# Kernel optimization log

Measured on AMD Instinct MI355X. Metric: run time of the kernel, lower is better.

## Reference

```python
import jax, jax.numpy as jnp
from jax import lax
import numpy as np

CHI, CHO = 256, 256
B, H, W = 4, 64, 64
KH = KW = 3
K = KH * KW
EPS = 1e-5


def setup_inputs() -> dict:
    key = jax.random.key(0)
    ks = jax.random.split(key, 8)
    x = jax.random.normal(ks[0], (B, CHI, H, W), jnp.float32)
    # offset/mask conv: chi -> 3*K channels (dy[K], dx[K], mask[K]); small init so offsets stay local
    w_off = jax.random.normal(ks[1], (3 * K, CHI, KH, KW), jnp.float32) * 0.01
    b_off = jax.random.normal(ks[2], (3 * K,), jnp.float32) * 0.01
    weight = jax.random.normal(ks[3], (CHO, CHI, KH, KW), jnp.float32) * 0.05
    bias = jax.random.normal(ks[4], (CHO,), jnp.float32) * 0.05
    gamma = 1.0 + 0.1 * jax.random.normal(ks[5], (CHO,), jnp.float32)
    beta = 0.1 * jax.random.normal(ks[6], (CHO,), jnp.float32)
    rmean = 0.1 * jax.random.normal(ks[7], (CHO,), jnp.float32)
    rvar = jnp.ones((CHO,), jnp.float32)
    return {"x": x, "w_off": w_off, "b_off": b_off, "weight": weight,
            "bias": bias, "gamma": gamma, "beta": beta, "rmean": rmean, "rvar": rvar}


def _dcn_bn_relu(x, w_off, b_off, weight, bias, gamma, beta, rmean, rvar):
    Bn, C, Hn, Wn = x.shape
    cho = weight.shape[0]
    # offset/mask branch: ordinary 3x3 same conv
    om = lax.conv_general_dilated(x, w_off, (1, 1), ((1, 1), (1, 1)),
                                  dimension_numbers=("NCHW", "OIHW", "NCHW"))
    om = om + b_off[None, :, None, None]
    o1, o2, m = jnp.split(om, 3, axis=1)            # each [B,K,H,W]
    mask = jax.nn.sigmoid(m).transpose(0, 2, 3, 1)  # [B,H,W,K]
    dy = o1.transpose(0, 2, 3, 1)                   # [B,H,W,K]
    dx = o2.transpose(0, 2, 3, 1)
    # sampling coords: p = out_pos - pad + k*dil + offset (stride=1, pad=1, dil=1)
    ky = jnp.repeat(jnp.arange(KH, dtype=x.dtype) - 1.0, KW)  # [K]
    kx = jnp.tile(jnp.arange(KW, dtype=x.dtype) - 1.0, KH)
    py = jnp.arange(Hn, dtype=x.dtype)[None, :, None, None] + ky + dy  # [B,H,W,K]
    px = jnp.arange(Wn, dtype=x.dtype)[None, None, :, None] + kx + dx

    xt = x.transpose(0, 2, 3, 1)  # [B,H,W,C]
    y0 = jnp.floor(py)
    x0 = jnp.floor(px)
    ly = py - y0
    lx = px - x0
    y0i = y0.astype(jnp.int32)
    x0i = x0.astype(jnp.int32)

    def corner(yi, xi, w):
        valid = (yi >= 0) & (yi < Hn) & (xi >= 0) & (xi < Wn)
        yc = jnp.clip(yi, 0, Hn - 1)
        xc = jnp.clip(xi, 0, Wn - 1)
        v = jax.vmap(lambda img, a, b: img[a, b])(xt, yc, xc)  # [B,H,W,K,C]
        return v * (w * valid.astype(x.dtype))[..., None]

    val = (corner(y0i, x0i, (1 - ly) * (1 - lx))
           + corner(y0i, x0i + 1, (1 - ly) * lx)
           + corner(y0i + 1, x0i, ly * (1 - lx))
           + corner(y0i + 1, x0i + 1, ly * lx))  # [B,H,W,K,C]

    cols = val * mask[..., None]  # modulated columns [B,H,W,K,C]
    wk = weight.reshape(cho, weight.shape[1], K)  # [O,C,K]
    out = jnp.einsum("bhwkc,ock->bohw", cols, wk) + bias[None, :, None, None]
    # BatchNorm (eval: running stats) + ReLU
    inv = gamma * lax.rsqrt(rvar + EPS)
    out = out * inv[None, :, None, None] + (beta - rmean * inv)[None, :, None, None]
    return jax.nn.relu(out)


def reference(x, w_off, b_off, weight, bias, gamma, beta, rmean, rvar):
    return _dcn_bn_relu(x, w_off, b_off, weight, bias, gamma, beta, rmean, rvar)
```

## Files before the change

kernel.cpp:

```cpp
#include <hip/hip_runtime.h>
#include <math.h>

#define NH 64
#define NW 64
#define NB 4
#define CHI 256
#define CHO 256
#define XT_B (66 * 66 * 256)

typedef __attribute__((ext_vector_type(8))) short bf16x8;
typedef __attribute__((ext_vector_type(4))) float f32x4;

static __device__ __forceinline__ unsigned short f2bf(float f) {
    unsigned int u = __float_as_uint(f);
    u += 0x7fffu + ((u >> 16) & 1u);
    return (unsigned short)(u >> 16);
}
static __device__ __forceinline__ float bflo(unsigned int p) { return __uint_as_float(p << 16); }
static __device__ __forceinline__ float bfhi(unsigned int p) { return __uint_as_float(p & 0xffff0000u); }
static __device__ __forceinline__ unsigned int pkbf(float a, float b) {
    unsigned int r;
    asm("v_cvt_pk_bf16_f32 %0, %1, %2" : "=v"(r) : "v"(a), "v"(b));
    return r;
}

#define BAR_LGKM() asm volatile("s_waitcnt lgkmcnt(0)\n\ts_barrier" ::: "memory")


__global__ __launch_bounds__(256) void prep_all(const float* __restrict__ weight,
                                                const float* __restrict__ w_off,
                                                const float* __restrict__ x,
                                                unsigned short* __restrict__ wB,
                                                unsigned short* __restrict__ wOB,
                                                unsigned short* __restrict__ xT) {
    __shared__ unsigned short sT[64 * 134];
    int bid = blockIdx.x, tid = threadIdx.x;
    if (bid < 2304) {
        int idx = bid * 256 + tid;
        int kin = idx & 31, o = (idx >> 5) & 255, ks = idx >> 13;
        int cc = ks / 9, kt = ks - cc * 9;
        int c = cc * 32 + kin;
        wB[idx] = f2bf(weight[((size_t)o * CHI + c) * 9 + kt]);
    } else if (bid < 2592) {
        int idx = (bid - 2304) * 256 + tid;
        int kin = idx & 31, oc = (idx >> 5) & 31, ks = idx >> 10;
        int cc = ks / 9, kt = ks - cc * 9;
        int c = cc * 32 + kin;
        wOB[idx] = (oc < 27) ? f2bf(w_off[((size_t)oc * CHI + c) * 9 + kt])
                             : (unsigned short)0;
    } else if (bid < 3104) {
        int bid2 = bid - 2592;
        int b = bid2 >> 7, rem = bid2 & 127;
        int y = rem >> 1, chalf = rem & 1;
        int c0 = chalf * 128;
        for (int rep = 0; rep < 8; ++rep) {
            int idx = rep * 256 + tid;
            int c = idx >> 4, p4 = (idx & 15) * 4;
            const float* src = x + (((size_t)b * CHI + c0 + c) * 64 + y) * 64 + p4;
            float4 v = *(const float4*)src;
            sT[(p4 + 0) * 134 + c] = f2bf(v.x);
            sT[(p4 + 1) * 134 + c] = f2bf(v.y);
            sT[(p4 + 2) * 134 + c] = f2bf(v.z);
            sT[(p4 + 3) * 134 + c] = f2bf(v.w);
        }
        __syncthreads();
        unsigned int* dst = (unsigned int*)(xT + ((size_t)(b * 66 + y + 1) * 66 + 1) * 256)
                          + chalf * 64;
        for (int rep = 0; rep < 16; ++rep) {
            int idx = rep * 256 + tid;
            int px = idx >> 6, cu = idx & 63;
            unsigned int lo = sT[px * 134 + cu * 2];
            unsigned int hi = sT[px * 134 + cu * 2 + 1];
            dst[(size_t)px * 128 + cu] = lo | (hi << 16);
        }
    } else {
        int flat = (bid - 3104) * 256 + tid;
        int b = flat / 33280, r = flat - b * 33280;
        unsigned int* xtu = (unsigned int*)xT;
        size_t base = (size_t)b * 66 * 66 * 128;
        size_t idx;
        if (r < 8448) {
            idx = base + r;
        } else if (r < 16896) {
            idx = base + (size_t)65 * 66 * 128 + (r - 8448);
        } else {
            int rc = r - 16896;
            int side = rc >> 13;
            int row = 1 + ((rc & 8191) >> 7);
            int cu = rc & 127;
            idx = base + ((size_t)row * 66 + (side ? 65 : 0)) * 128 + cu;
        }
        xtu[idx] = 0;
    }
}

__global__ __launch_bounds__(512, 4) void dcn_fused(
        const unsigned short* __restrict__ xT,
        const unsigned short* __restrict__ wOB,
        const unsigned short* __restrict__ wB,
        const float* __restrict__ b_off,
        const float* __restrict__ bias, const float* __restrict__ gamma,
        const float* __restrict__ beta, const float* __restrict__ rmean,
        const float* __restrict__ rvar, float* __restrict__ out) {
    __shared__ __align__(16) unsigned char smem[33280];
    int4*   s_po = (int4*)smem;
    float4* s_cw = (float4*)(smem + 4608);
    unsigned short* sA = (unsigned short*)(smem + 9216);
    float* sOff = (float*)(smem + 9216);
    float (*sOut)[260] = (float(*)[260])smem;

    int id = blockIdx.x;
    int xcd = id & 7, sl = id >> 3;
    int b = xcd >> 1;
    int h = (xcd & 1) * 32 + (sl & 31);
    int pxbase = (sl >> 5) * 32;

    int tid = threadIdx.x;
    int lane = tid & 63, q = tid >> 6;
    int ln = lane & 15, lk = lane >> 4;
    int nb = q & 3, kh = q >> 2;

    const unsigned short* xTfull = xT + (size_t)b * XT_B;
    const bf16x8* wOBv = (const bf16x8*)wOB;
    const bf16x8* wBv  = (const bf16x8*)wB;

    {
        int omt = q & 1, ont = (q >> 1) & 1, okq = q >> 2;
        int opx = pxbase + omt * 16 + ln;
        int oposbase = (h + 1) * 66 + opx + 1;
        f32x4 oa0 = {0.f, 0.f, 0.f, 0.f}, oa1 = {0.f, 0.f, 0.f, 0.f};
        for (int cc = okq * 4; cc < okq * 4 + 4; ++cc) {
#pragma unroll
            for (int kt = 0; kt < 9; ++kt) {
                int pos = oposbase + (kt / 3 - 1) * 66 + (kt % 3 - 1);
                bf16x8 af = *(const bf16x8*)&xTfull[(size_t)pos * 256 + cc * 32 + lk * 8];
                bf16x8 bo = wOBv[((size_t)(cc * 9 + kt) * 32 + ont * 16 + ln) * 4 + lk];
                if (kt & 1) oa1 = __builtin_amdgcn_mfma_f32_16x16x32_bf16(af, bo, oa1, 0, 0, 0);
                else        oa0 = __builtin_amdgcn_mfma_f32_16x16x32_bf16(af, bo, oa0, 0, 0, 0);
            }
        }
#pragma unroll
        for (int r = 0; r < 4; ++r)
            sOff[(okq * 32 + omt * 16 + lk * 4 + r) * 33 + ont * 16 + ln] = oa0[r] + oa1[r];
    }
    BAR_LGKM();

    for (int p = tid; p < 288; p += 512) {
        int k = p >> 5, pwl = p & 31, pw = pxbase + pwl;
        float dy = sOff[pwl * 33 + k]        + sOff[(32 + pwl) * 33 + k]        + b_off[k];
        float dx = sOff[pwl * 33 + k + 9]    + sOff[(32 + pwl) * 33 + k + 9]    + b_off[k + 9];
        float mp = sOff[pwl * 33 + k + 18]   + sOff[(32 + pwl) * 33 + k + 18]   + b_off[k + 18];
        float mv = 1.f / (1.f + __expf(-mp));
        float py  = (float)h  + (float)(k / 3 - 1) + dy;
        float pxf = (float)pw + (float)(k % 3 - 1) + dx;
        float y0f = floorf(py), x0f = floorf(pxf);
        int y0 = (int)y0f, x0 = (int)x0f;
        float ly = py - y0f, lx = pxf - x0f;
        int y0c = min(max(y0, -1), 64), y1c = min(max(y0 + 1, -1), 64);
        int x0c = min(max(x0, -1), 64), x1c = min(max(x0 + 1, -1), 64);
        int ry0 = (y0c + 1) * 66, ry1 = (y1c + 1) * 66;
        s_po[p] = make_int4(ry0 + x0c + 1, ry0 + x1c + 1, ry1 + x0c + 1, ry1 + x1c + 1);
        s_cw[p] = make_float4((1.f - ly) * (1.f - lx) * mv, (1.f - ly) * lx * mv,
                              ly * (1.f - lx) * mv,         ly * lx * mv);
    }

    int cg8 = tid & 3, pxl = (tid >> 2) & 31, sl4 = tid >> 7;
    int khp = sl4 >> 1, ip = sl4 & 1;
    const unsigned short* xTb = xTfull + cg8 * 8;

    f32x4 zf = {0.f, 0.f, 0.f, 0.f};
    f32x4 acc[2][4] = {{zf, zf, zf, zf}, {zf, zf, zf, zf}};

    uint4 C00, C01, C10, C11;

#define LOADS(s) do { int s_ = (s); int cc_ = s_ / 9; int kt_ = s_ - cc_ * 9;  \
        int4 o4_ = s_po[kt_ * 32 + pxl];                                       \
        const unsigned short* cb_ = xTb + cc_ * 32;                            \
        C00 = *(const uint4*)(cb_ + (size_t)o4_.x * 256);                      \
        C01 = *(const uint4*)(cb_ + (size_t)o4_.y * 256);                      \
        C10 = *(const uint4*)(cb_ + (size_t)o4_.z * 256);                      \
        C11 = *(const uint4*)(cb_ + (size_t)o4_.w * 256);                      \
    } while (0)

#define WRITEA(s, buf) do { int s_ = (s); int kt_ = s_ - (s_ / 9) * 9;         \
        float4 w_ = s_cw[kt_ * 32 + pxl];                                      \
        uint4 pk_;                                                             \
        pk_.x = pkbf(w_.x*bflo(C00.x)+w_.y*bflo(C01.x)+w_.z*bflo(C10.x)+w_.w*bflo(C11.x), \
                     w_.x*bfhi(C00.x)+w_.y*bfhi(C01.x)+w_.z*bfhi(C10.x)+w_.w*bfhi(C11.x)); \
        pk_.y = pkbf(w_.x*bflo(C00.y)+w_.y*bflo(C01.y)+w_.z*bflo(C10.y)+w_.w*bflo(C11.y), \
                     w_.x*bfhi(C00.y)+w_.y*bfhi(C01.y)+w_.z*bfhi(C10.y)+w_.w*bfhi(C11.y)); \
        pk_.z = pkbf(w_.x*bflo(C00.z)+w_.y*bflo(C01.z)+w_.z*bflo(C10.z)+w_.w*bflo(C11.z), \
                     w_.x*bfhi(C00.z)+w_.y*bfhi(C01.z)+w_.z*bfhi(C10.z)+w_.w*bfhi(C11.z)); \
        pk_.w = pkbf(w_.x*bflo(C00.w)+w_.y*bflo(C01.w)+w_.z*bflo(C10.w)+w_.w*bflo(C11.w), \
                     w_.x*bfhi(C00.w)+w_.y*bfhi(C01.w)+w_.z*bfhi(C10.w)+w_.w*bfhi(C11.w)); \
        *(uint4*)&sA[(buf) * 1280 + pxl * 40 + cg8 * 8] = pk_;                 \
    } while (0)

    BAR_LGKM();

    LOADS(khp * 36 + ip);
    WRITEA(khp * 36 + ip, sl4);
    LOADS(khp * 36 + 2 + ip);
    bf16x8 bfE[4], bfO[4];
#pragma unroll
    for (int j = 0; j < 4; ++j) {
        bfE[j] = wBv[((size_t)(kh * 36 + 0) * 256 + nb * 64 + j * 16 + ln) * 4 + lk];
        bfO[j] = wBv[((size_t)(kh * 36 + 1) * 256 + nb * 64 + j * 16 + ln) * 4 + lk];
    }
    BAR_LGKM();

    for (int g = 0; g < 18; ++g) {
        if (g + 1 < 18) WRITEA(khp * 36 + 2 * (g + 1) + ip, ((g + 1) & 1) * 4 + sl4);
        if (g + 2 < 18) LOADS(khp * 36 + 2 * (g + 2) + ip);

        int bufb = (g & 1) * 4 + kh * 2;
        const unsigned short* pA0 = &sA[bufb * 1280];
        const unsigned short* pA1 = &sA[bufb * 1280 + 1280];
        bf16x8 a00 = *(const bf16x8*)&pA0[ln * 40 + lk * 8];
        bf16x8 a01 = *(const bf16x8*)&pA0[(16 + ln) * 40 + lk * 8];
        bf16x8 a10 = *(const bf16x8*)&pA1[ln * 40 + lk * 8];
        bf16x8 a11 = *(const bf16x8*)&pA1[(16 + ln) * 40 + lk * 8];

#pragma unroll
        for (int j = 0; j < 4; ++j) {
            acc[0][j] = __builtin_amdgcn_mfma_f32_16x16x32_bf16(a00, bfE[j], acc[0][j], 0, 0, 0);
            acc[1][j] = __builtin_amdgcn_mfma_f32_16x16x32_bf16(a01, bfE[j], acc[1][j], 0, 0, 0);
        }
        if (2 * g + 2 < 36) {
#pragma unroll
            for (int j = 0; j < 4; ++j)
                bfE[j] = wBv[((size_t)(kh * 36 + 2 * g + 2) * 256 + nb * 64 + j * 16 + ln) * 4 + lk];
        }
#pragma unroll
        for (int j = 0; j < 4; ++j) {
            acc[0][j] = __builtin_amdgcn_mfma_f32_16x16x32_bf16(a10, bfO[j], acc[0][j], 0, 0, 0);
            acc[1][j] = __builtin_amdgcn_mfma_f32_16x16x32_bf16(a11, bfO[j], acc[1][j], 0, 0, 0);
        }
        if (2 * g + 3 < 36) {
#pragma unroll
            for (int j = 0; j < 4; ++j)
                bfO[j] = wBv[((size_t)(kh * 36 + 2 * g + 3) * 256 + nb * 64 + j * 16 + ln) * 4 + lk];
        }
        BAR_LGKM();
    }
#undef LOADS
#undef WRITEA

    if (kh == 1) {
#pragma unroll
        for (int m = 0; m < 2; ++m)
#pragma unroll
            for (int j = 0; j < 4; ++j) {
                int oc = nb * 64 + j * 16 + ln;
#pragma unroll
                for (int r = 0; r < 4; ++r)
                    sOut[m * 16 + lk * 4 + r][oc] = acc[m][j][r];
            }
    }
    __syncthreads();
    if (kh == 0) {
#pragma unroll
        for (int j = 0; j < 4; ++j) {
            int oc = nb * 64 + j * 16 + ln;
            float inv = gamma[oc] * rsqrtf(rvar[oc] + 1e-5f);
            float sh  = beta[oc] - rmean[oc] * inv + bias[oc] * inv;
#pragma unroll
            for (int m = 0; m < 2; ++m) {
                int row = m * 16 + lk * 4;
                float4 rr;
                rr.x = fmaxf((acc[m][j][0] + sOut[row + 0][oc]) * inv + sh, 0.f);
                rr.y = fmaxf((acc[m][j][1] + sOut[row + 1][oc]) * inv + sh, 0.f);
                rr.z = fmaxf((acc[m][j][2] + sOut[row + 2][oc]) * inv + sh, 0.f);
                rr.w = fmaxf((acc[m][j][3] + sOut[row + 3][oc]) * inv + sh, 0.f);
                size_t oi = (((size_t)b * 256 + oc) * 64 + h) * 64 + pxbase + row;
                *(float4*)(out + oi) = rr;
            }
        }
    }
}

extern "C" void kernel_launch(void* const* d_in, const int* in_sizes, int n_in,
                              void* d_out, int out_size, void* d_ws, size_t ws_size,
                              hipStream_t stream) {
    const float* x      = (const float*)d_in[0];
    const float* w_off  = (const float*)d_in[1];
    const float* b_off  = (const float*)d_in[2];
    const float* weight = (const float*)d_in[3];
    const float* bias   = (const float*)d_in[4];
    const float* gamma  = (const float*)d_in[5];
    const float* beta   = (const float*)d_in[6];
    const float* rmean  = (const float*)d_in[7];
    const float* rvar   = (const float*)d_in[8];
    float* out = (float*)d_out;

    unsigned short* wB  = (unsigned short*)d_ws;
    unsigned short* wOB = wB + 589824;
    unsigned short* xT  = wOB + 73728;

    hipLaunchKernelGGL(prep_all, dim3(3624), dim3(256), 0, stream,
                       weight, w_off, x, wB, wOB, xT);
    hipLaunchKernelGGL(dcn_fused, dim3(512), dim3(512), 0, stream,
                       xT, wOB, wB, b_off, bias, gamma, beta, rmean, rvar, out);
}
```

Baseline: 155.9 us.

## Widen block tile to a full 64-pixel row to halve weight reloads

Each block now computes a whole output row (64 pixels) instead of 32, so the grid shrinks from 512 to 256 blocks and each wave holds a 4x4 accumulator tile, reusing every loaded weight fragment across twice as many pixels. The offset conv and sampling stages are reorganised to match, with 4-way K-split partial sums and doubled shared-memory staging (about 65 KB). This cuts global weight traffic per output, at the cost of more registers (launch bounds lowered to 2), larger LDS, and only 256 blocks, which may underfill the GPU's compute units.

```diff
diff --git a/kernel.cpp b/kernel.cpp
--- a/kernel.cpp
+++ b/kernel.cpp
@@ -94,7 +94,7 @@
     }
 }
 
-__global__ __launch_bounds__(512, 4) void dcn_fused(
+__global__ __launch_bounds__(512, 2) void dcn_fused(
         const unsigned short* __restrict__ xT,
         const unsigned short* __restrict__ wOB,
         const unsigned short* __restrict__ wB,
@@ -102,18 +102,17 @@
         const float* __restrict__ bias, const float* __restrict__ gamma,
         const float* __restrict__ beta, const float* __restrict__ rmean,
         const float* __restrict__ rvar, float* __restrict__ out) {
-    __shared__ __align__(16) unsigned char smem[33280];
+    __shared__ __align__(16) unsigned char smem[66560];
     int4*   s_po = (int4*)smem;
-    float4* s_cw = (float4*)(smem + 4608);
-    unsigned short* sA = (unsigned short*)(smem + 9216);
-    float* sOff = (float*)(smem + 9216);
+    float4* s_cw = (float4*)(smem + 9216);
+    unsigned short* sA = (unsigned short*)(smem + 18432);
+    float* sOff = (float*)(smem + 18432);
     float (*sOut)[260] = (float(*)[260])smem;
 
     int id = blockIdx.x;
     int xcd = id & 7, sl = id >> 3;
     int b = xcd >> 1;
-    int h = (xcd & 1) * 32 + (sl & 31);
-    int pxbase = (sl >> 5) * 32;
+    int h = (xcd & 1) * 32 + sl;
 
     int tid = threadIdx.x;
     int lane = tid & 63, q = tid >> 6;
@@ -125,34 +124,48 @@
     const bf16x8* wBv  = (const bf16x8*)wB;
 
     {
-        int omt = q & 1, ont = (q >> 1) & 1, okq = q >> 2;
-        int opx = pxbase + omt * 16 + ln;
-        int oposbase = (h + 1) * 66 + opx + 1;
-        f32x4 oa0 = {0.f, 0.f, 0.f, 0.f}, oa1 = {0.f, 0.f, 0.f, 0.f};
-        for (int cc = okq * 4; cc < okq * 4 + 4; ++cc) {
+        int omt = q & 1, okq = q >> 1;
+        int px0 = omt * 32 + ln;
+        int posb = (h + 1) * 66 + 1 + px0;
+        f32x4 oa00 = {0.f,0.f,0.f,0.f}, oa01 = {0.f,0.f,0.f,0.f};
+        f32x4 oa10 = {0.f,0.f,0.f,0.f}, oa11 = {0.f,0.f,0.f,0.f};
+        for (int cc = okq * 2; cc < okq * 2 + 2; ++cc) {
 #pragma unroll
             for (int kt = 0; kt < 9; ++kt) {
-                int pos = oposbase + (kt / 3 - 1) * 66 + (kt % 3 - 1);
-                bf16x8 af = *(const bf16x8*)&xTfull[(size_t)pos * 256 + cc * 32 + lk * 8];
-                bf16x8 bo = wOBv[((size_t)(cc * 9 + kt) * 32 + ont * 16 + ln) * 4 + lk];
-                if (kt & 1) oa1 = __builtin_amdgcn_mfma_f32_16x16x32_bf16(af, bo, oa1, 0, 0, 0);
-                else        oa0 = __builtin_amdgcn_mfma_f32_16x16x32_bf16(af, bo, oa0, 0, 0, 0);
+                int pos = posb + (kt / 3 - 1) * 66 + (kt % 3 - 1);
+                bf16x8 A0 = *(const bf16x8*)&xTfull[(size_t)pos * 256 + cc * 32 + lk * 8];
+                bf16x8 A1 = *(const bf16x8*)&xTfull[(size_t)(pos + 16) * 256 + cc * 32 + lk * 8];
+                bf16x8 B0 = wOBv[((size_t)(cc * 9 + kt) * 32 + ln) * 4 + lk];
+                bf16x8 B1 = wOBv[((size_t)(cc * 9 + kt) * 32 + 16 + ln) * 4 + lk];
+                oa00 = __builtin_amdgcn_mfma_f32_16x16x32_bf16(A0, B0, oa00, 0, 0, 0);
+                oa01 = __builtin_amdgcn_mfma_f32_16x16x32_bf16(A0, B1, oa01, 0, 0, 0);
+                oa10 = __builtin_amdgcn_mfma_f32_16x16x32_bf16(A1, B0, oa10, 0, 0, 0);
+                oa11 = __builtin_amdgcn_mfma_f32_16x16x32_bf16(A1, B1, oa11, 0, 0, 0);
             }
         }
 #pragma unroll
-        for (int r = 0; r < 4; ++r)
-            sOff[(okq * 32 + omt * 16 + lk * 4 + r) * 33 + ont * 16 + ln] = oa0[r] + oa1[r];
+        for (int r = 0; r < 4; ++r) {
+            int row0 = okq * 64 + omt * 32 + lk * 4 + r;
+            sOff[row0 * 33 + ln]            = oa00[r];
+            sOff[row0 * 33 + 16 + ln]       = oa01[r];
+            sOff[(row0 + 16) * 33 + ln]     = oa10[r];
+            sOff[(row0 + 16) * 33 + 16 + ln]= oa11[r];
+        }
     }
     BAR_LGKM();
 
-    for (int p = tid; p < 288; p += 512) {
-        int k = p >> 5, pwl = p & 31, pw = pxbase + pwl;
-        float dy = sOff[pwl * 33 + k]        + sOff[(32 + pwl) * 33 + k]        + b_off[k];
-        float dx = sOff[pwl * 33 + k + 9]    + sOff[(32 + pwl) * 33 + k + 9]    + b_off[k + 9];
-        float mp = sOff[pwl * 33 + k + 18]   + sOff[(32 + pwl) * 33 + k + 18]   + b_off[k + 18];
+    for (int p = tid; p < 576; p += 512) {
+        int k = p >> 6, pwl = p & 63;
+        float dy = b_off[k], dx = b_off[k + 9], mp = b_off[k + 18];
+#pragma unroll
+        for (int jq = 0; jq < 4; ++jq) {
+            dy += sOff[(jq * 64 + pwl) * 33 + k];
+            dx += sOff[(jq * 64 + pwl) * 33 + k + 9];
+            mp += sOff[(jq * 64 + pwl) * 33 + k + 18];
+        }
         float mv = 1.f / (1.f + __expf(-mp));
-        float py  = (float)h  + (float)(k / 3 - 1) + dy;
-        float pxf = (float)pw + (float)(k % 3 - 1) + dx;
+        float py  = (float)h   + (float)(k / 3 - 1) + dy;
+        float pxf = (float)pwl + (float)(k % 3 - 1) + dx;
         float y0f = floorf(py), x0f = floorf(pxf);
         int y0 = (int)y0f, x0 = (int)x0f;
         float ly = py - y0f, lx = pxf - x0f;
@@ -164,43 +177,49 @@
                               ly * (1.f - lx) * mv,         ly * lx * mv);
     }
 
-    int cg8 = tid & 3, pxl = (tid >> 2) & 31, sl4 = tid >> 7;
-    int khp = sl4 >> 1, ip = sl4 & 1;
+    int cg8 = tid & 3, pxl = (tid >> 2) & 63, khp = tid >> 8;
     const unsigned short* xTb = xTfull + cg8 * 8;
 
     f32x4 zf = {0.f, 0.f, 0.f, 0.f};
-    f32x4 acc[2][4] = {{zf, zf, zf, zf}, {zf, zf, zf, zf}};
-
-    uint4 C00, C01, C10, C11;
-
-#define LOADS(s) do { int s_ = (s); int cc_ = s_ / 9; int kt_ = s_ - cc_ * 9;  \
-        int4 o4_ = s_po[kt_ * 32 + pxl];                                       \
+    f32x4 acc[4][4] = {{zf,zf,zf,zf},{zf,zf,zf,zf},{zf,zf,zf,zf},{zf,zf,zf,zf}};
+
+    uint4 P0, P1, P2, P3;
+    uint4 Q0, Q1, Q2, Q3;
+
+#define LOADSET(s, A0_, A1_, A2_, A3_) do { int s_ = (s);                      \
+        int cc_ = s_ / 9; int kt_ = s_ - cc_ * 9;                              \
+        int4 o4_ = s_po[kt_ * 64 + pxl];                                       \
         const unsigned short* cb_ = xTb + cc_ * 32;                            \
-        C00 = *(const uint4*)(cb_ + (size_t)o4_.x * 256);                      \
-        C01 = *(const uint4*)(cb_ + (size_t)o4_.y * 256);                      \
-        C10 = *(const uint4*)(cb_ + (size_t)o4_.z * 256);                      \
-        C11 = *(const uint4*)(cb_ + (size_t)o4_.w * 256);                      \
+        A0_ = *(const uint4*)(cb_ + (size_t)o4_.x * 256);                      \
+        A1_ = *(const uint4*)(cb_ + (size_t)o4_.y * 256);                      \
+        A2_ = *(const uint4*)(cb_ + (size_t)o4_.z * 256);                      \
+        A3_ = *(const uint4*)(cb_ + (size_t)o4_.w * 256);                      \
     } while (0)
 
-#define WRITEA(s, buf) do { int s_ = (s); int kt_ = s_ - (s_ / 9) * 9;         \
-        float4 w_ = s_cw[kt_ * 32 + pxl];                                      \
+#define WRITESET(s, buf, A0_, A1_, A2_, A3_) do { int s_ = (s);                \
+        int kt_ = s_ - (s_ / 9) * 9;                                           \
+        float4 w_ = s_cw[kt_ * 64 + pxl];                                      \
         uint4 pk_;                                                             \
-        pk_.x = pkbf(w_.x*bflo(C00.x)+w_.y*bflo(C01.x)+w_.z*bflo(C10.x)+w_.w*bflo(C11.x), \
-                     w_.x*bfhi(C00.x)+w_.y*bfhi(C01.x)+w_.z*bfhi(C10.x)+w_.w*bfhi(C11.x)); \
-        pk_.y = pkbf(w_.x*bflo(C00.y)+w_.y*bflo(C01.y)+w_.z*bflo(C10.y)+w_.w*bflo(C11.y), \
-                     w_.x*bfhi(C00.y)+w_.y*bfhi(C01.y)+w_.z*bfhi(C10.y)+w_.w*bfhi(C11.y)); \
-        pk_.z = pkbf(w_.x*bflo(C00.z)+w_.y*bflo(C01.z)+w_.z*bflo(C10.z)+w_.w*bflo(C11.z), \
-                     w_.x*bfhi(C00.z)+w_.y*bfhi(C01.z)+w_.z*bfhi(C10.z)+w_.w*bfhi(C11.z)); \
-        pk_.w = pkbf(w_.x*bflo(C00.w)+w_.y*bflo(C01.w)+w_.z*bflo(C10.w)+w_.w*bflo(C11.w), \
-                     w_.x*bfhi(C00.w)+w_.y*bfhi(C01.w)+w_.z*bfhi(C10.w)+w_.w*bfhi(C11.w)); \
-        *(uint4*)&sA[(buf) * 1280 + pxl * 40 + cg8 * 8] = pk_;                 \
+        pk_.x = pkbf(w_.x*bflo(A0_.x)+w_.y*bflo(A1_.x)+w_.z*bflo(A2_.x)+w_.w*bflo(A3_.x), \
+                     w_.x*bfhi(A0_.x)+w_.y*bfhi(A1_.x)+w_.z*bfhi(A2_.x)+w_.w*bfhi(A3_.x)); \
+        pk_.y = pkbf(w_.x*bflo(A0_.y)+w_.y*bflo(A1_.y)+w_.z*bflo(A2_.y)+w_.w*bflo(A3_.y), \
+                     w_.x*bfhi(A0_.y)+w_.y*bfhi(A1_.y)+w_.z*bfhi(A2_.y)+w_.w*bfhi(A3_.y)); \
+        pk_.z = pkbf(w_.x*bflo(A0_.z)+w_.y*bflo(A1_.z)+w_.z*bflo(A2_.z)+w_.w*bflo(A3_.z), \
+                     w_.x*bfhi(A0_.z)+w_.y*bfhi(A1_.z)+w_.z*bfhi(A2_.z)+w_.w*bfhi(A3_.z)); \
+        pk_.w = pkbf(w_.x*bflo(A0_.w)+w_.y*bflo(A1_.w)+w_.z*bflo(A2_.w)+w_.w*bflo(A3_.w), \
+                     w_.x*bfhi(A0_.w)+w_.y*bfhi(A1_.w)+w_.z*bfhi(A2_.w)+w_.w*bfhi(A3_.w)); \
+        *(uint4*)&sA[(buf) * 2560 + pxl * 40 + cg8 * 8] = pk_;                 \
     } while (0)
 
     BAR_LGKM();
 
-    LOADS(khp * 36 + ip);
-    WRITEA(khp * 36 + ip, sl4);
-    LOADS(khp * 36 + 2 + ip);
+    LOADSET(khp * 36 + 0, P0, P1, P2, P3);
+    LOADSET(khp * 36 + 1, Q0, Q1, Q2, Q3);
+    WRITESET(khp * 36 + 0, khp * 2 + 0, P0, P1, P2, P3);
+    WRITESET(khp * 36 + 1, khp * 2 + 1, Q0, Q1, Q2, Q3);
+    LOADSET(khp * 36 + 2, P0, P1, P2, P3);
+    LOADSET(khp * 36 + 3, Q0, Q1, Q2, Q3);
+
     bf16x8 bfE[4], bfO[4];
 #pragma unroll
     for (int j = 0; j < 4; ++j) {
@@ -210,32 +229,40 @@
     BAR_LGKM();
 
     for (int g = 0; g < 18; ++g) {
-        if (g + 1 < 18) WRITEA(khp * 36 + 2 * (g + 1) + ip, ((g + 1) & 1) * 4 + sl4);
-        if (g + 2 < 18) LOADS(khp * 36 + 2 * (g + 2) + ip);
-
-        int bufb = (g & 1) * 4 + kh * 2;
-        const unsigned short* pA0 = &sA[bufb * 1280];
-        const unsigned short* pA1 = &sA[bufb * 1280 + 1280];
-        bf16x8 a00 = *(const bf16x8*)&pA0[ln * 40 + lk * 8];
-        bf16x8 a01 = *(const bf16x8*)&pA0[(16 + ln) * 40 + lk * 8];
-        bf16x8 a10 = *(const bf16x8*)&pA1[ln * 40 + lk * 8];
-        bf16x8 a11 = *(const bf16x8*)&pA1[(16 + ln) * 40 + lk * 8];
-
-#pragma unroll
-        for (int j = 0; j < 4; ++j) {
-            acc[0][j] = __builtin_amdgcn_mfma_f32_16x16x32_bf16(a00, bfE[j], acc[0][j], 0, 0, 0);
-            acc[1][j] = __builtin_amdgcn_mfma_f32_16x16x32_bf16(a01, bfE[j], acc[1][j], 0, 0, 0);
-        }
+        if (g + 1 < 18) {
+            int base = ((g + 1) & 1) * 4 + khp * 2;
+            WRITESET(khp * 36 + 2 * (g + 1),     base,     P0, P1, P2, P3);
+            WRITESET(khp * 36 + 2 * (g + 1) + 1, base + 1, Q0, Q1, Q2, Q3);
+        }
+        if (g + 2 < 18) {
+            LOADSET(khp * 36 + 2 * (g + 2),     P0, P1, P2, P3);
+            LOADSET(khp * 36 + 2 * (g + 2) + 1, Q0, Q1, Q2, Q3);
+        }
+
+        int slotb = (g & 1) * 4 + kh * 2;
+        const unsigned short* pA0 = &sA[slotb * 2560];
+        const unsigned short* pA1 = &sA[(slotb + 1) * 2560];
+        bf16x8 a0[4], a1[4];
+#pragma unroll
+        for (int m = 0; m < 4; ++m) a0[m] = *(const bf16x8*)&pA0[(m * 16 + ln) * 40 + lk * 8];
+#pragma unroll
+        for (int m = 0; m < 4; ++m) a1[m] = *(const bf16x8*)&pA1[(m * 16 + ln) * 40 + lk * 8];
+
+#pragma unroll
+        for (int m = 0; m < 4; ++m)
+#pragma unroll
+            for (int j = 0; j < 4; ++j)
+                acc[m][j] = __builtin_amdgcn_mfma_f32_16x16x32_bf16(a0[m], bfE[j], acc[m][j], 0, 0, 0);
         if (2 * g + 2 < 36) {
 #pragma unroll
             for (int j = 0; j < 4; ++j)
                 bfE[j] = wBv[((size_t)(kh * 36 + 2 * g + 2) * 256 + nb * 64 + j * 16 + ln) * 4 + lk];
         }
 #pragma unroll
-        for (int j = 0; j < 4; ++j) {
-            acc[0][j] = __builtin_amdgcn_mfma_f32_16x16x32_bf16(a10, bfO[j], acc[0][j], 0, 0, 0);
-            acc[1][j] = __builtin_amdgcn_mfma_f32_16x16x32_bf16(a11, bfO[j], acc[1][j], 0, 0, 0);
-        }
+        for (int m = 0; m < 4; ++m)
+#pragma unroll
+            for (int j = 0; j < 4; ++j)
+                acc[m][j] = __builtin_amdgcn_mfma_f32_16x16x32_bf16(a1[m], bfO[j], acc[m][j], 0, 0, 0);
         if (2 * g + 3 < 36) {
 #pragma unroll
             for (int j = 0; j < 4; ++j)
@@ -243,12 +270,12 @@
         }
         BAR_LGKM();
     }
-#undef LOADS
-#undef WRITEA
+#undef LOADSET
+#undef WRITESET
 
     if (kh == 1) {
 #pragma unroll
-        for (int m = 0; m < 2; ++m)
+        for (int m = 0; m < 4; ++m)
 #pragma unroll
             for (int j = 0; j < 4; ++j) {
                 int oc = nb * 64 + j * 16 + ln;
@@ -265,14 +292,14 @@
             float inv = gamma[oc] * rsqrtf(rvar[oc] + 1e-5f);
             float sh  = beta[oc] - rmean[oc] * inv + bias[oc] * inv;
 #pragma unroll
-            for (int m = 0; m < 2; ++m) {
+            for (int m = 0; m < 4; ++m) {
                 int row = m * 16 + lk * 4;
                 float4 rr;
                 rr.x = fmaxf((acc[m][j][0] + sOut[row + 0][oc]) * inv + sh, 0.f);
                 rr.y = fmaxf((acc[m][j][1] + sOut[row + 1][oc]) * inv + sh, 0.f);
                 rr.z = fmaxf((acc[m][j][2] + sOut[row + 2][oc]) * inv + sh, 0.f);
                 rr.w = fmaxf((acc[m][j][3] + sOut[row + 3][oc]) * inv + sh, 0.f);
-                size_t oi = (((size_t)b * 256 + oc) * 64 + h) * 64 + pxbase + row;
+                size_t oi = (((size_t)b * 256 + oc) * 64 + h) * 64 + row;
                 *(float4*)(out + oi) = rr;
             }
         }
@@ -299,6 +326,6 @@
 
     hipLaunchKernelGGL(prep_all, dim3(3624), dim3(256), 0, stream,
                        weight, w_off, x, wB, wOB, xT);
-    hipLaunchKernelGGL(dcn_fused, dim3(512), dim3(512), 0, stream,
+    hipLaunchKernelGGL(dcn_fused, dim3(256), dim3(512), 0, stream,
                        xT, wOB, wB, b_off, bias, gamma, beta, rmean, rvar, out);
 }
```

After: 138.7 us. 11.0% less time.
